# Kernel tuning notes

Hardware: AMD Instinct MI355X
Metric: run time of the kernel (lower is better)

## Reference

```python
import jax, jax.numpy as jnp
import numpy as np

B, IN, OUT = 8192, 4096, 4096


def setup_inputs() -> dict:
    key = jax.random.key(0)
    k_x, k_w, k_t, k_n = jax.random.split(key, 4)
    # int8 activations and weights (stored as int8; accumulated in int32)
    x = jax.random.randint(k_x, (B, IN), -128, 128, dtype=jnp.int32).astype(jnp.int8)
    W = jax.random.randint(k_w, (OUT, IN), -128, 128, dtype=jnp.int32).astype(jnp.int8)
    # per-channel BN fold: additive term t (int32) and negative bitshift n
    t = jax.random.randint(k_t, (OUT,), -(1 << 15), 1 << 15, dtype=jnp.int32)
    n = jax.random.randint(k_n, (OUT,), -9, -6, dtype=jnp.int32)  # shift right by 6..8
    act_min = jnp.full((OUT,), -128, dtype=jnp.int32)
    act_max = jnp.full((OUT,), 127, dtype=jnp.int32)
    return {"x": x, "W": W, "t": t, "n": n, "act_min": act_min, "act_max": act_max}


def reference(x, W, t, n, act_min, act_max):
    # int32-accumulate int8 GEMM: F.linear(x, W) -> [B, OUT]
    acc = jnp.matmul(x.astype(jnp.int32), W.astype(jnp.int32).T)
    acc = acc + t  # broadcast per-output-channel bias add
    acc = jnp.right_shift(acc, -n)  # arithmetic right shift requantization
    acc = jnp.clip(acc, act_min, act_max)
    # pure_positive is False (act_min < 0) -> cast to small signed type
    return acc.astype(jnp.int8)
```

## Files before the change

kernel.cpp:

```cpp
#include <hip/hip_runtime.h>
#include <stdint.h>


#define BDIM 8192
#define INDIM 4096
#define OUTDIM 4096

typedef __attribute__((ext_vector_type(4))) int I4;
typedef __attribute__((ext_vector_type(16))) int I16;

__global__ __launch_bounds__(256) void pack_frag32(const int* __restrict__ x,
                                                   const int* __restrict__ W,
                                                   uint32_t* __restrict__ xp,
                                                   uint32_t* __restrict__ wp) {
    const uint32_t xq = (BDIM / 32) * 128 * 64;
    uint32_t u = blockIdx.x * 256 + threadIdx.x;
    const int* src;
    uint32_t* dst;
    if (u < xq) {
        uint32_t m32 = u >> 13, kb = (u >> 6) & 127, lane = u & 63;
        src = x + (size_t)(m32 * 32 + (lane & 31)) * INDIM + kb * 32 + (lane >> 5) * 16;
        dst = xp + (size_t)u * 4;
    } else {
        uint32_t v = u - xq;
        uint32_t n32 = v >> 13, kb = (v >> 6) & 127, lane = v & 63;
        src = W + (size_t)(n32 * 32 + (lane & 31)) * INDIM + kb * 32 + (lane >> 5) * 16;
        dst = wp + (size_t)v * 4;
    }
    uint32_t ow[4];
#pragma unroll
    for (int q = 0; q < 4; ++q) {
        int4 a = ((const int4*)src)[q];
        ow[q] = ((uint32_t)a.x & 255u)
              | (((uint32_t)a.y & 255u) << 8)
              | (((uint32_t)a.z & 255u) << 16)
              | (((uint32_t)a.w & 255u) << 24);
    }
    *(uint4*)dst = *(uint4*)ow;
}

#define LOAD_SET(fa, fb, off)                                            \
    do {                                                                 \
        _Pragma("unroll")                                                \
        for (int i = 0; i < 4; ++i) fa[i] = *(const I4*)(pa[i] + (off)); \
        _Pragma("unroll")                                                \
        for (int j = 0; j < 4; ++j) fb[j] = *(const I4*)(pb[j] + (off)); \
    } while (0)

#define MFMA_SET(fa, fb)                                                 \
    do {                                                                 \
        _Pragma("unroll")                                                \
        for (int i = 0; i < 4; ++i)                                      \
            _Pragma("unroll")                                            \
            for (int j = 0; j < 4; ++j)                                  \
                acc[i][j] = __builtin_amdgcn_mfma_i32_32x32x32_i8(fa[i], fb[j], acc[i][j], 0, 0, 0); \
    } while (0)

__global__ __launch_bounds__(64, 1) void gemm_flat32(
    const uint8_t* __restrict__ Xp,
    const uint8_t* __restrict__ Wp,
    const int* __restrict__ t, const int* __restrict__ nsh,
    const int* __restrict__ amin, const int* __restrict__ amax,
    int* __restrict__ out) {

    const int bn = blockIdx.x;
    const int bm = blockIdx.y;
    const int lane = threadIdx.x;

    const uint8_t* pa[4];
    const uint8_t* pb[4];
#pragma unroll
    for (int i = 0; i < 4; ++i)
        pa[i] = Xp + ((size_t)(bm * 4 + i) << 17) + lane * 16;
#pragma unroll
    for (int j = 0; j < 4; ++j)
        pb[j] = Wp + ((size_t)(bn * 4 + j) << 17) + lane * 16;

    I16 acc[4][4];
#pragma unroll
    for (int i = 0; i < 4; ++i)
#pragma unroll
        for (int j = 0; j < 4; ++j)
#pragma unroll
            for (int r = 0; r < 16; ++r) acc[i][j][r] = 0;

    I4 a0[4], b0[4], a1[4], b1[4], a2[4], b2[4];
    LOAD_SET(a0, b0, 0);
    LOAD_SET(a1, b1, 1024);
    LOAD_SET(a2, b2, 2048);

#pragma unroll 1
    for (int kb = 0; kb < 123; kb += 3) {
        const size_t base = (size_t)kb * 1024;
        MFMA_SET(a0, b0);
        LOAD_SET(a0, b0, base + 3 * 1024);
        MFMA_SET(a1, b1);
        LOAD_SET(a1, b1, base + 4 * 1024);
        MFMA_SET(a2, b2);
        LOAD_SET(a2, b2, base + 5 * 1024);
    }
    MFMA_SET(a0, b0);
    LOAD_SET(a0, b0, (size_t)126 * 1024);
    MFMA_SET(a1, b1);
    LOAD_SET(a1, b1, (size_t)127 * 1024);
    MFMA_SET(a2, b2);
    MFMA_SET(a0, b0);
    MFMA_SET(a1, b1);

#pragma unroll
    for (int j = 0; j < 4; ++j) {
        const int o = bn * 128 + j * 32 + (lane & 31);
        const int tt = t[o];
        const int sh = -nsh[o];
        const int mn = amin[o];
        const int mx = amax[o];
#pragma unroll
        for (int i = 0; i < 4; ++i) {
            const int rowbase = bm * 128 + i * 32 + 4 * (lane >> 5);
#pragma unroll
            for (int r = 0; r < 16; ++r) {
                const int row = rowbase + (r & 3) + 8 * (r >> 2);
                int v = acc[i][j][r] + tt;
                v >>= sh;
                v = v < mn ? mn : (v > mx ? mx : v);
                __builtin_nontemporal_store(v, &out[(size_t)row * OUTDIM + o]);
            }
        }
    }
}

extern "C" void kernel_launch(void* const* d_in, const int* in_sizes, int n_in,
                              void* d_out, int out_size, void* d_ws, size_t ws_size,
                              hipStream_t stream) {
    const int* x = (const int*)d_in[0];
    const int* W = (const int*)d_in[1];
    const int* t = (const int*)d_in[2];
    const int* n = (const int*)d_in[3];
    const int* amin = (const int*)d_in[4];
    const int* amax = (const int*)d_in[5];
    int* out = (int*)d_out;

    uint8_t* xp = (uint8_t*)d_ws;
    uint8_t* wp = xp + (size_t)BDIM * INDIM;

    {
        int nthreads = (BDIM / 32) * 128 * 64 + (OUTDIM / 32) * 128 * 64;
        pack_frag32<<<nthreads / 256, 256, 0, stream>>>(x, W, (uint32_t*)xp, (uint32_t*)wp);
    }

    dim3 grid(OUTDIM / 128, BDIM / 128);
    gemm_flat32<<<grid, 64, 0, stream>>>(xp, wp, t, n, amin, amax, out);
}
```

Before: 388.5 us.

## Stage fragments through LDS with 256x256 block tiles and coalesced pack

```diff
diff --git a/kernel.cpp b/kernel.cpp
--- a/kernel.cpp
+++ b/kernel.cpp
@@ -9,54 +9,93 @@
 typedef __attribute__((ext_vector_type(4))) int I4;
 typedef __attribute__((ext_vector_type(16))) int I16;
 
-__global__ __launch_bounds__(256) void pack_frag32(const int* __restrict__ x,
-                                                   const int* __restrict__ W,
-                                                   uint32_t* __restrict__ xp,
-                                                   uint32_t* __restrict__ wp) {
-    const uint32_t xq = (BDIM / 32) * 128 * 64;
-    uint32_t u = blockIdx.x * 256 + threadIdx.x;
+__global__ __launch_bounds__(256) void pack_lds(const int* __restrict__ x,
+                                                const int* __restrict__ W,
+                                                uint32_t* __restrict__ xp,
+                                                uint32_t* __restrict__ wp) {
+    __shared__ uint32_t sb[8192];
+    const int tid = threadIdx.x;
+    const int bid = blockIdx.x;
     const int* src;
     uint32_t* dst;
-    if (u < xq) {
-        uint32_t m32 = u >> 13, kb = (u >> 6) & 127, lane = u & 63;
-        src = x + (size_t)(m32 * 32 + (lane & 31)) * INDIM + kb * 32 + (lane >> 5) * 16;
-        dst = xp + (size_t)u * 4;
+    if (bid < 1024) {
+        const int m32 = bid >> 2, q = bid & 3;
+        src = x + (size_t)m32 * 32 * INDIM + q * 1024;
+        dst = xp + (size_t)m32 * 32768 + q * 8192;
     } else {
-        uint32_t v = u - xq;
-        uint32_t n32 = v >> 13, kb = (v >> 6) & 127, lane = v & 63;
-        src = W + (size_t)(n32 * 32 + (lane & 31)) * INDIM + kb * 32 + (lane >> 5) * 16;
-        dst = wp + (size_t)v * 4;
-    }
-    uint32_t ow[4];
-#pragma unroll
-    for (int q = 0; q < 4; ++q) {
-        int4 a = ((const int4*)src)[q];
-        ow[q] = ((uint32_t)a.x & 255u)
-              | (((uint32_t)a.y & 255u) << 8)
-              | (((uint32_t)a.z & 255u) << 16)
-              | (((uint32_t)a.w & 255u) << 24);
-    }
-    *(uint4*)dst = *(uint4*)ow;
-}
-
-#define LOAD_SET(fa, fb, off)                                            \
-    do {                                                                 \
-        _Pragma("unroll")                                                \
-        for (int i = 0; i < 4; ++i) fa[i] = *(const I4*)(pa[i] + (off)); \
-        _Pragma("unroll")                                                \
-        for (int j = 0; j < 4; ++j) fb[j] = *(const I4*)(pb[j] + (off)); \
-    } while (0)
-
-#define MFMA_SET(fa, fb)                                                 \
-    do {                                                                 \
-        _Pragma("unroll")                                                \
-        for (int i = 0; i < 4; ++i)                                      \
-            _Pragma("unroll")                                            \
-            for (int j = 0; j < 4; ++j)                                  \
-                acc[i][j] = __builtin_amdgcn_mfma_i32_32x32x32_i8(fa[i], fb[j], acc[i][j], 0, 0, 0); \
-    } while (0)
-
-__global__ __launch_bounds__(64, 1) void gemm_flat32(
+        const int v = bid - 1024;
+        const int n32 = v >> 2, q = v & 3;
+        src = W + (size_t)n32 * 32 * INDIM + q * 1024;
+        dst = wp + (size_t)n32 * 32768 + q * 8192;
+    }
+    const int kb_l = tid >> 3;
+    const int lane_hi = ((tid >> 2) & 1) << 5;
+    const int bslot = tid & 3;
+#pragma unroll 4
+    for (int rr = 0; rr < 32; ++rr) {
+        int4 a = *(const int4*)(src + (size_t)rr * INDIM + tid * 4);
+        uint32_t v = ((uint32_t)a.x & 255u) | (((uint32_t)a.y & 255u) << 8)
+                   | (((uint32_t)a.z & 255u) << 16) | (((uint32_t)a.w & 255u) << 24);
+        uint32_t idx = (uint32_t)(kb_l * 256 + (rr + lane_hi) * 4 + bslot);
+        idx ^= ((idx >> 8) & 7u) << 2;
+        sb[idx] = v;
+    }
+    __syncthreads();
+#pragma unroll
+    for (int it = 0; it < 8; ++it) {
+        uint32_t idx = (uint32_t)(it * 1024 + tid * 4);
+        idx ^= ((idx >> 8) & 7u) << 2;
+        uint4 vv = *(const uint4*)&sb[idx];
+        *(uint4*)(dst + it * 1024 + tid * 4) = vv;
+    }
+}
+
+__device__ __forceinline__ void glds16(const void* g, void* l) {
+    __builtin_amdgcn_global_load_lds((__attribute__((address_space(1))) void*)g,
+                                     (__attribute__((address_space(3))) void*)l,
+                                     16, 0, 0);
+}
+
+#define VMW8() asm volatile("s_waitcnt vmcnt(8)" ::: "memory")
+#define VMW4() asm volatile("s_waitcnt vmcnt(4)" ::: "memory")
+#define VMW0() asm volatile("s_waitcnt vmcnt(0)" ::: "memory")
+#define BARRIER()                          \
+    do {                                   \
+        __builtin_amdgcn_s_barrier();      \
+        asm volatile("" ::: "memory");     \
+    } while (0)
+#define SCHEDB() __builtin_amdgcn_sched_barrier(0)
+
+#define STAGE(SETK, BUF)                                                          \
+    do {                                                                          \
+        _Pragma("unroll")                                                         \
+        for (int i_ = 0; i_ < 4; ++i_)                                            \
+            glds16(gsrc[i_] + (size_t)(SETK) * 1024,                              \
+                   lds_raw + (BUF) * 16384 + (w * 4 + i_) * 1024);                \
+    } while (0)
+
+#define FRAG_READ(FA, FB, BUF)                                                    \
+    do {                                                                          \
+        const uint8_t* lb_ = lds_raw + (BUF) * 16384 + lane * 16;                 \
+        _Pragma("unroll")                                                         \
+        for (int i_ = 0; i_ < 4; ++i_)                                            \
+            FA[i_] = *(const I4*)(lb_ + (wr4 + i_) * 1024);                       \
+        _Pragma("unroll")                                                         \
+        for (int j_ = 0; j_ < 4; ++j_)                                            \
+            FB[j_] = *(const I4*)(lb_ + 8192 + (wc4 + j_) * 1024);                \
+    } while (0)
+
+#define MFMA_SET(FA, FB)                                                          \
+    do {                                                                          \
+        _Pragma("unroll")                                                         \
+        for (int i_ = 0; i_ < 4; ++i_)                                            \
+            _Pragma("unroll")                                                     \
+            for (int j_ = 0; j_ < 4; ++j_)                                        \
+                acc[i_][j_] = __builtin_amdgcn_mfma_i32_32x32x32_i8(              \
+                    FA[i_], FB[j_], acc[i_][j_], 0, 0, 0);                        \
+    } while (0)
+
+__global__ __launch_bounds__(256, 1) void gemm_lds(
     const uint8_t* __restrict__ Xp,
     const uint8_t* __restrict__ Wp,
     const int* __restrict__ t, const int* __restrict__ nsh,
@@ -65,58 +104,89 @@
 
     const int bn = blockIdx.x;
     const int bm = blockIdx.y;
-    const int lane = threadIdx.x;
-
-    const uint8_t* pa[4];
-    const uint8_t* pb[4];
+    const int tid = threadIdx.x;
+    const int lane = tid & 63;
+    const int w = tid >> 6;
+    const int wr = w >> 1;
+    const int wc = w & 1;
+    const int wr4 = wr * 4;
+    const int wc4 = wc * 4;
+
+    __shared__ uint8_t lds_raw[65536];
+
+    const uint8_t* gsrc[4];
+#pragma unroll
+    for (int i = 0; i < 4; ++i) {
+        const int s = w * 4 + i;
+        gsrc[i] = (s < 8) ? Xp + ((size_t)(bm * 8 + s) << 17) + lane * 16
+                          : Wp + ((size_t)(bn * 8 + (s - 8)) << 17) + lane * 16;
+    }
+
+    I16 acc[4][4];
 #pragma unroll
     for (int i = 0; i < 4; ++i)
-        pa[i] = Xp + ((size_t)(bm * 4 + i) << 17) + lane * 16;
-#pragma unroll
-    for (int j = 0; j < 4; ++j)
-        pb[j] = Wp + ((size_t)(bn * 4 + j) << 17) + lane * 16;
-
-    I16 acc[4][4];
-#pragma unroll
-    for (int i = 0; i < 4; ++i)
 #pragma unroll
         for (int j = 0; j < 4; ++j)
 #pragma unroll
             for (int r = 0; r < 16; ++r) acc[i][j][r] = 0;
 
-    I4 a0[4], b0[4], a1[4], b1[4], a2[4], b2[4];
-    LOAD_SET(a0, b0, 0);
-    LOAD_SET(a1, b1, 1024);
-    LOAD_SET(a2, b2, 2048);
+    I4 a0[4], b0[4], a1[4], b1[4];
+
+    STAGE(0, 0);
+    STAGE(1, 1);
+    STAGE(2, 2);
+    VMW8();
+    BARRIER();
+    FRAG_READ(a0, b0, 0);
 
 #pragma unroll 1
-    for (int kb = 0; kb < 123; kb += 3) {
-        const size_t base = (size_t)kb * 1024;
+    for (int kk = 0; kk < 124; kk += 4) {
+        VMW4(); BARRIER();
+        STAGE(kk + 3, 3);
+        FRAG_READ(a1, b1, 1);
         MFMA_SET(a0, b0);
-        LOAD_SET(a0, b0, base + 3 * 1024);
+        SCHEDB();
+        VMW4(); BARRIER();
+        STAGE(kk + 4, 0);
+        FRAG_READ(a0, b0, 2);
         MFMA_SET(a1, b1);
-        LOAD_SET(a1, b1, base + 4 * 1024);
-        MFMA_SET(a2, b2);
-        LOAD_SET(a2, b2, base + 5 * 1024);
-    }
+        SCHEDB();
+        VMW4(); BARRIER();
+        STAGE(kk + 5, 1);
+        FRAG_READ(a1, b1, 3);
+        MFMA_SET(a0, b0);
+        SCHEDB();
+        VMW4(); BARRIER();
+        STAGE(kk + 6, 2);
+        FRAG_READ(a0, b0, 0);
+        MFMA_SET(a1, b1);
+        SCHEDB();
+    }
+    VMW4(); BARRIER();
+    STAGE(127, 3);
+    FRAG_READ(a1, b1, 1);
     MFMA_SET(a0, b0);
-    LOAD_SET(a0, b0, (size_t)126 * 1024);
+    SCHEDB();
+    VMW4(); BARRIER();
+    FRAG_READ(a0, b0, 2);
     MFMA_SET(a1, b1);
-    LOAD_SET(a1, b1, (size_t)127 * 1024);
-    MFMA_SET(a2, b2);
+    SCHEDB();
+    VMW0(); BARRIER();
+    FRAG_READ(a1, b1, 3);
     MFMA_SET(a0, b0);
+    SCHEDB();
     MFMA_SET(a1, b1);
 
 #pragma unroll
     for (int j = 0; j < 4; ++j) {
-        const int o = bn * 128 + j * 32 + (lane & 31);
+        const int o = bn * 256 + wc4 * 32 + j * 32 + (lane & 31);
         const int tt = t[o];
         const int sh = -nsh[o];
         const int mn = amin[o];
         const int mx = amax[o];
 #pragma unroll
         for (int i = 0; i < 4; ++i) {
-            const int rowbase = bm * 128 + i * 32 + 4 * (lane >> 5);
+            const int rowbase = bm * 256 + wr4 * 32 + i * 32 + 4 * (lane >> 5);
 #pragma unroll
             for (int r = 0; r < 16; ++r) {
                 const int row = rowbase + (r & 3) + 8 * (r >> 2);
@@ -143,11 +213,8 @@
     uint8_t* xp = (uint8_t*)d_ws;
     uint8_t* wp = xp + (size_t)BDIM * INDIM;
 
-    {
-        int nthreads = (BDIM / 32) * 128 * 64 + (OUTDIM / 32) * 128 * 64;
-        pack_frag32<<<nthreads / 256, 256, 0, stream>>>(x, W, (uint32_t*)xp, (uint32_t*)wp);
-    }
-
-    dim3 grid(OUTDIM / 128, BDIM / 128);
-    gemm_flat32<<<grid, 64, 0, stream>>>(xp, wp, t, n, amin, amax, out);
-}
+    pack_lds<<<1536, 256, 0, stream>>>(x, W, (uint32_t*)xp, (uint32_t*)wp);
+
+    dim3 grid(OUTDIM / 256, BDIM / 256);
+    gemm_lds<<<grid, 256, 0, stream>>>(xp, wp, t, n, amin, amax, out);
+}
```

Result: no change. 394.8 us (+1.6%).
